# Kernel tuning notes

Hardware: AMD Instinct MI355X
Metric: run time of the kernel (lower is better)

Reference implementation:

```python
import jax, jax.numpy as jnp
import numpy as np

L = 2048      # seq_len
E = 2048      # hidden_dim
H = 16        # num_heads
D = E // H    # head_dim


def setup_inputs() -> dict:
    key = jax.random.key(0)
    ks = jax.random.split(key, 6)
    x = jax.random.normal(ks[0], (L, E), dtype=jnp.float32)
    bias_matrix = jax.random.normal(ks[1], (L, L), dtype=jnp.float32) * 0.1
    # nn.MultiheadAttention params: packed in_proj [3E, E] + bias [3E], out_proj [E, E] + bias [E]
    in_proj_weight = jax.random.normal(ks[2], (3 * E, E), dtype=jnp.float32) * 0.02
    in_proj_bias = jax.random.normal(ks[3], (3 * E,), dtype=jnp.float32) * 0.02
    out_proj_weight = jax.random.normal(ks[4], (E, E), dtype=jnp.float32) * 0.02
    out_proj_bias = jax.random.normal(ks[5], (E,), dtype=jnp.float32) * 0.02
    return {
        "x": x,
        "bias_matrix": bias_matrix,
        "in_proj_weight": in_proj_weight,
        "in_proj_bias": in_proj_bias,
        "out_proj_weight": out_proj_weight,
        "out_proj_bias": out_proj_bias,
    }


def reference(x, bias_matrix, in_proj_weight, in_proj_bias, out_proj_weight, out_proj_bias):
    # Packed QKV projection (torch Linear convention: y = x @ W.T + b)
    qkv = x @ in_proj_weight.T + in_proj_bias            # [L, 3E]
    q, k, v = jnp.split(qkv, 3, axis=-1)                 # each [L, E]
    q = q.reshape(L, H, D)
    k = k.reshape(L, H, D)
    v = v.reshape(L, H, D)
    scale = 1.0 / jnp.sqrt(jnp.asarray(D, dtype=x.dtype))
    # scores: [H, L, L]; bias_matrix broadcast over heads (torch 2D attn_mask semantics)
    scores = jnp.einsum("lhd,mhd->hlm", q * scale, k) + bias_matrix[None, :, :]
    attn = jax.nn.softmax(scores, axis=-1)
    ctx = jnp.einsum("hlm,mhd->lhd", attn, v).reshape(L, E)
    out = ctx @ out_proj_weight.T + out_proj_bias        # [L, E]
    return out
```

## Files before the change

### kernel.cpp

```cpp
#include <hip/hip_runtime.h>
#include <math.h>

#define L_SEQ 2048
#define E_DIM 2048
#define H_NUM 16
#define D_HEAD 128

typedef __attribute__((ext_vector_type(8))) _Float16 half8;
typedef __attribute__((ext_vector_type(4))) _Float16 half4;
typedef __attribute__((ext_vector_type(4))) float floatx4;

static __device__ __forceinline__ void gload16(const void* g, void* lds) {
  __builtin_amdgcn_global_load_lds(
      (const __attribute__((address_space(1))) void*)g,
      (__attribute__((address_space(3))) void*)lds, 16, 0, 0);
}

__global__ __launch_bounds__(256)
void cvt3_f32_f16(const float* __restrict__ a, _Float16* __restrict__ oa, int na,
                  const float* __restrict__ b, _Float16* __restrict__ ob, int nb,
                  const float* __restrict__ c, _Float16* __restrict__ oc, int nc) {
  int i = (blockIdx.x * 256 + threadIdx.x) * 8;
  const float* src;
  _Float16* dst;
  if (i < na) {
    src = a + i; dst = oa + i;
  } else if (i < na + nb) {
    src = b + (i - na); dst = ob + (i - na);
  } else if (i < na + nb + nc) {
    src = c + (i - na - nb); dst = oc + (i - na - nb);
  } else {
    return;
  }
  float4 p = *(const float4*)src;
  float4 q = *(const float4*)(src + 4);
  half8 h = {(_Float16)p.x, (_Float16)p.y, (_Float16)p.z, (_Float16)p.w,
             (_Float16)q.x, (_Float16)q.y, (_Float16)q.z, (_Float16)q.w};
  *(half8*)dst = h;
}

template <int TM, int TN, int WR, int WC, int EPI>
__global__ __launch_bounds__(256)
void gemm_mfma(const _Float16* __restrict__ A, const _Float16* __restrict__ B,
               const float* __restrict__ bias, float* __restrict__ C,
               _Float16* __restrict__ qk, _Float16* __restrict__ vt,
               int M, int N, int K) {
  constexpr int RT = TM / (16 * WR);
  constexpr int CT = TN / (16 * WC);
  constexpr int ACH = TM / 8;
  constexpr int NCH = (TM + TN) / 32;

  __shared__ _Float16 As[2][TM * 64];
  __shared__ _Float16 Bs[2][TN * 64];

  const int tid = threadIdx.x;
  const int wave = tid >> 6, lane = tid & 63;
  const int l15 = lane & 15, quad = lane >> 4;
  const int wr = wave / WC, wc = wave % WC;
  const int row0 = blockIdx.y * TM, col0 = blockIdx.x * TN;

  const int srow = lane >> 3;
  const int gc = (lane & 7) ^ srow;

  auto stage = [&](int buf, int k0) {
#pragma unroll
    for (int c = 0; c < NCH; ++c) {
      int chunk = wave * NCH + c;
      if (chunk < ACH) {
        int row = chunk * 8 + srow;
        gload16((const char*)(A + (size_t)(row0 + row) * K + k0) + gc * 16,
                (char*)&As[buf][0] + chunk * 1024);
      } else {
        int bch = chunk - ACH;
        int row = bch * 8 + srow;
        gload16((const char*)(B + (size_t)(col0 + row) * K + k0) + gc * 16,
                (char*)&Bs[buf][0] + bch * 1024);
      }
    }
  };

  floatx4 acc[RT][CT];
#pragma unroll
  for (int i = 0; i < RT; ++i)
#pragma unroll
    for (int j = 0; j < CT; ++j) acc[i][j] = (floatx4){0.f, 0.f, 0.f, 0.f};

  const int niter = K / 64;
  stage(0, 0);

  for (int it = 0; it < niter; ++it) {
    const int cur = it & 1;
    __syncthreads();
    if (it + 1 < niter) stage(cur ^ 1, (it + 1) * 64);

#pragma unroll
    for (int ks = 0; ks < 2; ++ks) {
      half8 af[RT], bf[CT];
#pragma unroll
      for (int t = 0; t < RT; ++t) {
        int r = wr * (16 * RT) + t * 16 + l15;
        af[t] = *(const half8*)&As[cur][r * 64 + (((ks * 4 + quad) ^ (r & 7)) * 8)];
      }
#pragma unroll
      for (int t = 0; t < CT; ++t) {
        int r = wc * (16 * CT) + t * 16 + l15;
        bf[t] = *(const half8*)&Bs[cur][r * 64 + (((ks * 4 + quad) ^ (r & 7)) * 8)];
      }
#pragma unroll
      for (int tr = 0; tr < RT; ++tr)
#pragma unroll
        for (int tc = 0; tc < CT; ++tc)
          acc[tr][tc] = __builtin_amdgcn_mfma_f32_16x16x32_f16(
              af[tr], bf[tc], acc[tr][tc], 0, 0, 0);
    }
  }

  const int crow = row0 + wr * (16 * RT);
  const int ccol = col0 + wc * (16 * CT);

  if (EPI == 0) {
#pragma unroll
    for (int tc = 0; tc < CT; ++tc) {
      int col = ccol + tc * 16 + l15;
      float bb = bias[col];
#pragma unroll
      for (int tr = 0; tr < RT; ++tr)
#pragma unroll
        for (int r = 0; r < 4; ++r)
          C[(size_t)(crow + tr * 16 + quad * 4 + r) * N + col] =
              acc[tr][tc][r] + bb;
    }
  } else if (col0 < 2 * E_DIM) {
#pragma unroll
    for (int tc = 0; tc < CT; ++tc) {
      int col = ccol + tc * 16 + l15;
      float bb = bias[col];
#pragma unroll
      for (int tr = 0; tr < RT; ++tr)
#pragma unroll
        for (int r = 0; r < 4; ++r)
          qk[(size_t)(crow + tr * 16 + quad * 4 + r) * (2 * E_DIM) + col] =
              (_Float16)(acc[tr][tc][r] + bb);
    }
  } else {
#pragma unroll
    for (int tc = 0; tc < CT; ++tc) {
      int col = ccol + tc * 16 + l15;
      float bb = bias[col];
      int vrow = col - 2 * E_DIM;
#pragma unroll
      for (int tr = 0; tr < RT; ++tr) {
        int rbase = crow + tr * 16 + quad * 4;
        half4 h = {(_Float16)(acc[tr][tc][0] + bb), (_Float16)(acc[tr][tc][1] + bb),
                   (_Float16)(acc[tr][tc][2] + bb), (_Float16)(acc[tr][tc][3] + bb)};
        *(half4*)&vt[(size_t)vrow * L_SEQ + rbase] = h;
      }
    }
  }
}

__global__ __launch_bounds__(256, 1)
void attn_mfma(const _Float16* __restrict__ qk, const _Float16* __restrict__ vt,
               const float* __restrict__ bias, _Float16* __restrict__ ctx) {
  const int h = blockIdx.x;
  const int q0 = blockIdx.y * 128;
  const int tid = threadIdx.x;
  const int wave = tid >> 6;
  const int lane = tid & 63;
  const int l15 = lane & 15;
  const int quad = lane >> 4;

  __shared__ _Float16 Ks[2][64][136];
  __shared__ _Float16 Vst[2][128][72];
  __shared__ _Float16 Ps[128][72];

  half8 qa[2][4];
#pragma unroll
  for (int rt = 0; rt < 2; ++rt) {
    const _Float16* qp = qk + (size_t)(q0 + wave * 32 + rt * 16 + l15) * (2 * E_DIM) +
                         h * D_HEAD + quad * 8;
#pragma unroll
    for (int ks = 0; ks < 4; ++ks) qa[rt][ks] = *(const half8*)(qp + ks * 32);
  }

  float l_i[2] = {0.f, 0.f};
  floatx4 o[2][8];
#pragma unroll
  for (int rt = 0; rt < 2; ++rt)
#pragma unroll
    for (int t = 0; t < 8; ++t) o[rt][t] = (floatx4){0.f, 0.f, 0.f, 0.f};

  const float scale = 0.088388347648318447f;

  half8 kreg[4], vreg[4];
  floatx4 bcur[2][4], bnxt[2][4];
#pragma unroll
  for (int c = 0; c < 4; ++c) {
    int m = c * 256 + tid;
    kreg[c] = *(const half8*)(qk + (size_t)(m >> 4) * (2 * E_DIM) + E_DIM +
                              h * D_HEAD + (m & 15) * 8);
    vreg[c] = *(const half8*)(vt + (size_t)(h * D_HEAD + (m >> 3)) * L_SEQ +
                              (m & 7) * 8);
  }
#pragma unroll
  for (int rt = 0; rt < 2; ++rt)
#pragma unroll
    for (int t = 0; t < 4; ++t)
      bcur[rt][t] = *(const floatx4*)&bias[(size_t)(q0 + wave * 32 + rt * 16 + l15) *
                                               L_SEQ + 16 * t + quad * 4];
#pragma unroll
  for (int c = 0; c < 4; ++c) {
    int m = c * 256 + tid;
    *(half8*)&Ks[0][m >> 4][(m & 15) * 8] = kreg[c];
    *(half8*)&Vst[0][m >> 3][(m & 7) * 8] = vreg[c];
  }

#pragma unroll 2
  for (int it = 0; it < 32; ++it) {
    const int cur = it & 1, nxt = cur ^ 1;
    const int kt = it * 64;
    __syncthreads();

    if (it < 31) {
#pragma unroll
      for (int c = 0; c < 4; ++c) {
        int m = c * 256 + tid;
        kreg[c] = *(const half8*)(qk + (size_t)(kt + 64 + (m >> 4)) * (2 * E_DIM) +
                                  E_DIM + h * D_HEAD + (m & 15) * 8);
        vreg[c] = *(const half8*)(vt + (size_t)(h * D_HEAD + (m >> 3)) * L_SEQ +
                                  kt + 64 + (m & 7) * 8);
      }
#pragma unroll
      for (int rt = 0; rt < 2; ++rt)
#pragma unroll
        for (int t = 0; t < 4; ++t)
          bnxt[rt][t] =
              *(const floatx4*)&bias[(size_t)(q0 + wave * 32 + rt * 16 + l15) *
                                         L_SEQ + kt + 64 + 16 * t + quad * 4];
    }

    floatx4 st[2][4];
#pragma unroll
    for (int t = 0; t < 4; ++t) {
      st[0][t] = (floatx4){0.f, 0.f, 0.f, 0.f};
      st[1][t] = (floatx4){0.f, 0.f, 0.f, 0.f};
    }
#pragma unroll
    for (int ks = 0; ks < 4; ++ks)
#pragma unroll
      for (int t = 0; t < 4; ++t) {
        half8 kf = *(const half8*)&Ks[cur][16 * t + l15][ks * 32 + quad * 8];
        st[0][t] = __builtin_amdgcn_mfma_f32_16x16x32_f16(kf, qa[0][ks], st[0][t], 0, 0, 0);
        st[1][t] = __builtin_amdgcn_mfma_f32_16x16x32_f16(kf, qa[1][ks], st[1][t], 0, 0, 0);
      }

#pragma unroll
    for (int rt = 0; rt < 2; ++rt) {
      float ls = 0.f;
      float ps[4][4];
#pragma unroll
      for (int t = 0; t < 4; ++t)
#pragma unroll
        for (int r = 0; r < 4; ++r) {
          float p = __expf(fmaf(st[rt][t][r], scale, bcur[rt][t][r]));
          ps[t][r] = p;
          ls += p;
        }
      ls += __shfl_xor(ls, 16);
      ls += __shfl_xor(ls, 32);
      l_i[rt] += ls;
#pragma unroll
      for (int t = 0; t < 4; ++t) {
        half4 hp = {(_Float16)ps[t][0], (_Float16)ps[t][1],
                    (_Float16)ps[t][2], (_Float16)ps[t][3]};
        *(half4*)&Ps[wave * 32 + rt * 16 + l15][16 * t + quad * 4] = hp;
      }
    }

    half8 pa[2][2];
#pragma unroll
    for (int rt = 0; rt < 2; ++rt)
#pragma unroll
      for (int ks = 0; ks < 2; ++ks)
        pa[rt][ks] = *(const half8*)&Ps[wave * 32 + rt * 16 + l15][ks * 32 + quad * 8];
#pragma unroll
    for (int t = 0; t < 8; ++t) {
#pragma unroll
      for (int ks = 0; ks < 2; ++ks) {
        half8 vf = *(const half8*)&Vst[cur][16 * t + l15][ks * 32 + quad * 8];
        o[0][t] = __builtin_amdgcn_mfma_f32_16x16x32_f16(pa[0][ks], vf, o[0][t], 0, 0, 0);
        o[1][t] = __builtin_amdgcn_mfma_f32_16x16x32_f16(pa[1][ks], vf, o[1][t], 0, 0, 0);
      }
    }

    if (it < 31) {
#pragma unroll
      for (int c = 0; c < 4; ++c) {
        int m = c * 256 + tid;
        *(half8*)&Ks[nxt][m >> 4][(m & 15) * 8] = kreg[c];
        *(half8*)&Vst[nxt][m >> 3][(m & 7) * 8] = vreg[c];
      }
#pragma unroll
      for (int rt = 0; rt < 2; ++rt)
#pragma unroll
        for (int t = 0; t < 4; ++t) bcur[rt][t] = bnxt[rt][t];
    }
  }

#pragma unroll
  for (int rt = 0; rt < 2; ++rt) {
    float inv[4];
#pragma unroll
    for (int r = 0; r < 4; ++r) inv[r] = 1.f / __shfl(l_i[rt], quad * 4 + r);
#pragma unroll
    for (int t = 0; t < 8; ++t)
#pragma unroll
      for (int r = 0; r < 4; ++r) {
        int row = q0 + wave * 32 + rt * 16 + quad * 4 + r;
        ctx[(size_t)row * E_DIM + h * D_HEAD + 16 * t + l15] =
            (_Float16)(o[rt][t][r] * inv[r]);
      }
  }
}

extern "C" void kernel_launch(void* const* d_in, const int* in_sizes, int n_in,
                              void* d_out, int out_size, void* d_ws, size_t ws_size,
                              hipStream_t stream) {
  const float* x          = (const float*)d_in[0];
  const float* bias_mat   = (const float*)d_in[1];
  const float* in_proj_w  = (const float*)d_in[2];
  const float* in_proj_b  = (const float*)d_in[3];
  const float* out_proj_w = (const float*)d_in[4];
  const float* out_proj_b = (const float*)d_in[5];
  float* out = (float*)d_out;

  _Float16* x16 = (_Float16*)d_ws;
  _Float16* w1  = x16 + (size_t)L_SEQ * E_DIM;
  _Float16* w2  = w1 + (size_t)3 * E_DIM * E_DIM;
  _Float16* qk  = w2 + (size_t)E_DIM * E_DIM;
  _Float16* vt  = qk + (size_t)L_SEQ * 2 * E_DIM;
  _Float16* ctx = vt + (size_t)E_DIM * L_SEQ;

  dim3 blk(256);
  const int nx = L_SEQ * E_DIM, nw1 = 3 * E_DIM * E_DIM, nw2 = E_DIM * E_DIM;

  cvt3_f32_f16<<<(nx + nw1 + nw2) / 2048, blk, 0, stream>>>(
      x, x16, nx, in_proj_w, w1, nw1, out_proj_w, w2, nw2);

  gemm_mfma<128, 128, 2, 2, 1><<<dim3(3 * E_DIM / 128, L_SEQ / 128), blk, 0, stream>>>(
      x16, w1, in_proj_b, nullptr, qk, vt, L_SEQ, 3 * E_DIM, E_DIM);

  attn_mfma<<<dim3(H_NUM, L_SEQ / 128), blk, 0, stream>>>(qk, vt, bias_mat, ctx);

  gemm_mfma<128, 64, 4, 1, 0><<<dim3(E_DIM / 64, L_SEQ / 128), blk, 0, stream>>>(
      ctx, w2, out_proj_b, out, nullptr, nullptr, L_SEQ, E_DIM, E_DIM);
}
```

Measured before the change: 285.4 us.

## Fuse fp32-to-fp16 conversion into GEMM loads and use 8-wave attention blocks

Drops the separate conversion kernel. The GEMMs now load fp32 inputs into registers and convert them to fp16 as they write to LDS, with the register loads prefetched across the MFMA loop. The attention kernel goes from 4 to 8 waves per block, each wave owning 16 query rows instead of 32, so more waves share each K/V tile. The cost is fp32 global reads of the weights inside the GEMM tiles (twice the bytes, read repeatedly across tiles) instead of a single conversion pass, and register-path staging in place of async direct-to-LDS loads.

```diff
diff --git a/kernel.cpp b/kernel.cpp
--- a/kernel.cpp
+++ b/kernel.cpp
@@ -16,32 +16,9 @@
       (__attribute__((address_space(3))) void*)lds, 16, 0, 0);
 }
 
-__global__ __launch_bounds__(256)
-void cvt3_f32_f16(const float* __restrict__ a, _Float16* __restrict__ oa, int na,
-                  const float* __restrict__ b, _Float16* __restrict__ ob, int nb,
-                  const float* __restrict__ c, _Float16* __restrict__ oc, int nc) {
-  int i = (blockIdx.x * 256 + threadIdx.x) * 8;
-  const float* src;
-  _Float16* dst;
-  if (i < na) {
-    src = a + i; dst = oa + i;
-  } else if (i < na + nb) {
-    src = b + (i - na); dst = ob + (i - na);
-  } else if (i < na + nb + nc) {
-    src = c + (i - na - nb); dst = oc + (i - na - nb);
-  } else {
-    return;
-  }
-  float4 p = *(const float4*)src;
-  float4 q = *(const float4*)(src + 4);
-  half8 h = {(_Float16)p.x, (_Float16)p.y, (_Float16)p.z, (_Float16)p.w,
-             (_Float16)q.x, (_Float16)q.y, (_Float16)q.z, (_Float16)q.w};
-  *(half8*)dst = h;
-}
-
-template <int TM, int TN, int WR, int WC, int EPI>
-__global__ __launch_bounds__(256)
-void gemm_mfma(const _Float16* __restrict__ A, const _Float16* __restrict__ B,
+template <int TM, int TN, int WR, int WC, int EPI, int CVTA, int CVTB>
+__global__ __launch_bounds__(256, 2)
+void gemm_mfma(const void* __restrict__ Ap, const void* __restrict__ Bp,
                const float* __restrict__ bias, float* __restrict__ C,
                _Float16* __restrict__ qk, _Float16* __restrict__ vt,
                int M, int N, int K) {
@@ -50,6 +27,11 @@
   constexpr int ACH = TM / 8;
   constexpr int NCH = (TM + TN) / 32;
 
+  const _Float16* A16 = (const _Float16*)Ap;
+  const float*    A32 = (const float*)Ap;
+  const _Float16* B16 = (const _Float16*)Bp;
+  const float*    B32 = (const float*)Bp;
+
   __shared__ _Float16 As[2][TM * 64];
   __shared__ _Float16 Bs[2][TN * 64];
 
@@ -62,22 +44,64 @@
   const int srow = lane >> 3;
   const int gc = (lane & 7) ^ srow;
 
-  auto stage = [&](int buf, int k0) {
+  float4 sreg[NCH][2];
+
+  auto loadRegs = [&](int k0) {
 #pragma unroll
     for (int c = 0; c < NCH; ++c) {
       int chunk = wave * NCH + c;
       if (chunk < ACH) {
-        int row = chunk * 8 + srow;
-        gload16((const char*)(A + (size_t)(row0 + row) * K + k0) + gc * 16,
-                (char*)&As[buf][0] + chunk * 1024);
+        if (CVTA) {
+          int row = chunk * 8 + srow;
+          const float* p = A32 + (size_t)(row0 + row) * K + k0 + gc * 8;
+          sreg[c][0] = *(const float4*)p;
+          sreg[c][1] = *(const float4*)(p + 4);
+        }
       } else {
-        int bch = chunk - ACH;
-        int row = bch * 8 + srow;
-        gload16((const char*)(B + (size_t)(col0 + row) * K + k0) + gc * 16,
-                (char*)&Bs[buf][0] + bch * 1024);
+        if (CVTB) {
+          int row = (chunk - ACH) * 8 + srow;
+          const float* p = B32 + (size_t)(col0 + row) * K + k0 + gc * 8;
+          sreg[c][0] = *(const float4*)p;
+          sreg[c][1] = *(const float4*)(p + 4);
+        }
       }
     }
   };
+  auto issueAsync = [&](int buf, int k0) {
+#pragma unroll
+    for (int c = 0; c < NCH; ++c) {
+      int chunk = wave * NCH + c;
+      if (chunk < ACH) {
+        if (!CVTA) {
+          int row = chunk * 8 + srow;
+          gload16((const char*)(A16 + (size_t)(row0 + row) * K + k0) + gc * 16,
+                  (char*)&As[buf][0] + chunk * 1024);
+        }
+      } else {
+        if (!CVTB) {
+          int row = (chunk - ACH) * 8 + srow;
+          gload16((const char*)(B16 + (size_t)(col0 + row) * K + k0) + gc * 16,
+                  (char*)&Bs[buf][0] + (chunk - ACH) * 1024);
+        }
+      }
+    }
+  };
+  auto writeRegs = [&](int buf) {
+#pragma unroll
+    for (int c = 0; c < NCH; ++c) {
+      int chunk = wave * NCH + c;
+      bool docvt = (chunk < ACH) ? (CVTA != 0) : (CVTB != 0);
+      if (docvt) {
+        float4 a = sreg[c][0], b = sreg[c][1];
+        half8 h = {(_Float16)a.x, (_Float16)a.y, (_Float16)a.z, (_Float16)a.w,
+                   (_Float16)b.x, (_Float16)b.y, (_Float16)b.z, (_Float16)b.w};
+        char* base = (chunk < ACH)
+                         ? (char*)&As[buf][0] + chunk * 1024
+                         : (char*)&Bs[buf][0] + (chunk - ACH) * 1024;
+        *(half8*)(base + lane * 16) = h;
+      }
+    }
+  };
 
   floatx4 acc[RT][CT];
 #pragma unroll
@@ -86,12 +110,17 @@
     for (int j = 0; j < CT; ++j) acc[i][j] = (floatx4){0.f, 0.f, 0.f, 0.f};
 
   const int niter = K / 64;
-  stage(0, 0);
+  loadRegs(0);
+  issueAsync(0, 0);
+  writeRegs(0);
 
   for (int it = 0; it < niter; ++it) {
     const int cur = it & 1;
     __syncthreads();
-    if (it + 1 < niter) stage(cur ^ 1, (it + 1) * 64);
+    if (it + 1 < niter) {
+      loadRegs((it + 1) * 64);
+      issueAsync(cur ^ 1, (it + 1) * 64);
+    }
 
 #pragma unroll
     for (int ks = 0; ks < 2; ++ks) {
@@ -113,6 +142,8 @@
           acc[tr][tc] = __builtin_amdgcn_mfma_f32_16x16x32_f16(
               af[tr], bf[tc], acc[tr][tc], 0, 0, 0);
     }
+
+    if (it + 1 < niter) writeRegs(cur ^ 1);
   }
 
   const int crow = row0 + wr * (16 * RT);
@@ -159,7 +190,7 @@
   }
 }
 
-__global__ __launch_bounds__(256, 1)
+__global__ __launch_bounds__(512, 2)
 void attn_mfma(const _Float16* __restrict__ qk, const _Float16* __restrict__ vt,
                const float* __restrict__ bias, _Float16* __restrict__ ctx) {
   const int h = blockIdx.x;
@@ -174,43 +205,38 @@
   __shared__ _Float16 Vst[2][128][72];
   __shared__ _Float16 Ps[128][72];
 
-  half8 qa[2][4];
-#pragma unroll
-  for (int rt = 0; rt < 2; ++rt) {
-    const _Float16* qp = qk + (size_t)(q0 + wave * 32 + rt * 16 + l15) * (2 * E_DIM) +
+  half8 qa[4];
+  {
+    const _Float16* qp = qk + (size_t)(q0 + wave * 16 + l15) * (2 * E_DIM) +
                          h * D_HEAD + quad * 8;
 #pragma unroll
-    for (int ks = 0; ks < 4; ++ks) qa[rt][ks] = *(const half8*)(qp + ks * 32);
-  }
-
-  float l_i[2] = {0.f, 0.f};
-  floatx4 o[2][8];
-#pragma unroll
-  for (int rt = 0; rt < 2; ++rt)
-#pragma unroll
-    for (int t = 0; t < 8; ++t) o[rt][t] = (floatx4){0.f, 0.f, 0.f, 0.f};
+    for (int ks = 0; ks < 4; ++ks) qa[ks] = *(const half8*)(qp + ks * 32);
+  }
+
+  float l_i = 0.f;
+  floatx4 o[8];
+#pragma unroll
+  for (int t = 0; t < 8; ++t) o[t] = (floatx4){0.f, 0.f, 0.f, 0.f};
 
   const float scale = 0.088388347648318447f;
 
-  half8 kreg[4], vreg[4];
-  floatx4 bcur[2][4], bnxt[2][4];
-#pragma unroll
-  for (int c = 0; c < 4; ++c) {
-    int m = c * 256 + tid;
+  half8 kreg[2], vreg[2];
+  floatx4 bcur[4], bnxt[4];
+#pragma unroll
+  for (int c = 0; c < 2; ++c) {
+    int m = c * 512 + tid;
     kreg[c] = *(const half8*)(qk + (size_t)(m >> 4) * (2 * E_DIM) + E_DIM +
                               h * D_HEAD + (m & 15) * 8);
     vreg[c] = *(const half8*)(vt + (size_t)(h * D_HEAD + (m >> 3)) * L_SEQ +
                               (m & 7) * 8);
   }
 #pragma unroll
-  for (int rt = 0; rt < 2; ++rt)
-#pragma unroll
-    for (int t = 0; t < 4; ++t)
-      bcur[rt][t] = *(const floatx4*)&bias[(size_t)(q0 + wave * 32 + rt * 16 + l15) *
-                                               L_SEQ + 16 * t + quad * 4];
-#pragma unroll
-  for (int c = 0; c < 4; ++c) {
-    int m = c * 256 + tid;
+  for (int t = 0; t < 4; ++t)
+    bcur[t] = *(const floatx4*)&bias[(size_t)(q0 + wave * 16 + l15) * L_SEQ +
+                                    16 * t + quad * 4];
+#pragma unroll
+  for (int c = 0; c < 2; ++c) {
+    int m = c * 512 + tid;
     *(half8*)&Ks[0][m >> 4][(m & 15) * 8] = kreg[c];
     *(half8*)&Vst[0][m >> 3][(m & 7) * 8] = vreg[c];
   }
@@ -223,104 +249,87 @@
 
     if (it < 31) {
 #pragma unroll
-      for (int c = 0; c < 4; ++c) {
-        int m = c * 256 + tid;
+      for (int c = 0; c < 2; ++c) {
+        int m = c * 512 + tid;
         kreg[c] = *(const half8*)(qk + (size_t)(kt + 64 + (m >> 4)) * (2 * E_DIM) +
                                   E_DIM + h * D_HEAD + (m & 15) * 8);
         vreg[c] = *(const half8*)(vt + (size_t)(h * D_HEAD + (m >> 3)) * L_SEQ +
                                   kt + 64 + (m & 7) * 8);
       }
 #pragma unroll
-      for (int rt = 0; rt < 2; ++rt)
-#pragma unroll
-        for (int t = 0; t < 4; ++t)
-          bnxt[rt][t] =
-              *(const floatx4*)&bias[(size_t)(q0 + wave * 32 + rt * 16 + l15) *
-                                         L_SEQ + kt + 64 + 16 * t + quad * 4];
-    }
-
-    floatx4 st[2][4];
-#pragma unroll
-    for (int t = 0; t < 4; ++t) {
-      st[0][t] = (floatx4){0.f, 0.f, 0.f, 0.f};
-      st[1][t] = (floatx4){0.f, 0.f, 0.f, 0.f};
-    }
+      for (int t = 0; t < 4; ++t)
+        bnxt[t] = *(const floatx4*)&bias[(size_t)(q0 + wave * 16 + l15) * L_SEQ +
+                                         kt + 64 + 16 * t + quad * 4];
+    }
+
+    floatx4 st[4];
+#pragma unroll
+    for (int t = 0; t < 4; ++t) st[t] = (floatx4){0.f, 0.f, 0.f, 0.f};
 #pragma unroll
     for (int ks = 0; ks < 4; ++ks)
 #pragma unroll
       for (int t = 0; t < 4; ++t) {
         half8 kf = *(const half8*)&Ks[cur][16 * t + l15][ks * 32 + quad * 8];
-        st[0][t] = __builtin_amdgcn_mfma_f32_16x16x32_f16(kf, qa[0][ks], st[0][t], 0, 0, 0);
-        st[1][t] = __builtin_amdgcn_mfma_f32_16x16x32_f16(kf, qa[1][ks], st[1][t], 0, 0, 0);
-      }
-
-#pragma unroll
-    for (int rt = 0; rt < 2; ++rt) {
+        st[t] = __builtin_amdgcn_mfma_f32_16x16x32_f16(kf, qa[ks], st[t], 0, 0, 0);
+      }
+
+    {
       float ls = 0.f;
       float ps[4][4];
 #pragma unroll
       for (int t = 0; t < 4; ++t)
 #pragma unroll
         for (int r = 0; r < 4; ++r) {
-          float p = __expf(fmaf(st[rt][t][r], scale, bcur[rt][t][r]));
+          float p = __expf(fmaf(st[t][r], scale, bcur[t][r]));
           ps[t][r] = p;
           ls += p;
         }
       ls += __shfl_xor(ls, 16);
       ls += __shfl_xor(ls, 32);
-      l_i[rt] += ls;
+      l_i += ls;
 #pragma unroll
       for (int t = 0; t < 4; ++t) {
         half4 hp = {(_Float16)ps[t][0], (_Float16)ps[t][1],
                     (_Float16)ps[t][2], (_Float16)ps[t][3]};
-        *(half4*)&Ps[wave * 32 + rt * 16 + l15][16 * t + quad * 4] = hp;
-      }
-    }
-
-    half8 pa[2][2];
-#pragma unroll
-    for (int rt = 0; rt < 2; ++rt)
-#pragma unroll
-      for (int ks = 0; ks < 2; ++ks)
-        pa[rt][ks] = *(const half8*)&Ps[wave * 32 + rt * 16 + l15][ks * 32 + quad * 8];
-#pragma unroll
-    for (int t = 0; t < 8; ++t) {
+        *(half4*)&Ps[wave * 16 + l15][16 * t + quad * 4] = hp;
+      }
+    }
+
+    half8 pa[2];
+#pragma unroll
+    for (int ks = 0; ks < 2; ++ks)
+      pa[ks] = *(const half8*)&Ps[wave * 16 + l15][ks * 32 + quad * 8];
+#pragma unroll
+    for (int t = 0; t < 8; ++t)
 #pragma unroll
       for (int ks = 0; ks < 2; ++ks) {
         half8 vf = *(const half8*)&Vst[cur][16 * t + l15][ks * 32 + quad * 8];
-        o[0][t] = __builtin_amdgcn_mfma_f32_16x16x32_f16(pa[0][ks], vf, o[0][t], 0, 0, 0);
-        o[1][t] = __builtin_amdgcn_mfma_f32_16x16x32_f16(pa[1][ks], vf, o[1][t], 0, 0, 0);
-      }
-    }
+        o[t] = __builtin_amdgcn_mfma_f32_16x16x32_f16(pa[ks], vf, o[t], 0, 0, 0);
+      }
 
     if (it < 31) {
 #pragma unroll
-      for (int c = 0; c < 4; ++c) {
-        int m = c * 256 + tid;
+      for (int c = 0; c < 2; ++c) {
+        int m = c * 512 + tid;
         *(half8*)&Ks[nxt][m >> 4][(m & 15) * 8] = kreg[c];
         *(half8*)&Vst[nxt][m >> 3][(m & 7) * 8] = vreg[c];
       }
 #pragma unroll
-      for (int rt = 0; rt < 2; ++rt)
-#pragma unroll
-        for (int t = 0; t < 4; ++t) bcur[rt][t] = bnxt[rt][t];
-    }
-  }
-
-#pragma unroll
-  for (int rt = 0; rt < 2; ++rt) {
-    float inv[4];
-#pragma unroll
-    for (int r = 0; r < 4; ++r) inv[r] = 1.f / __shfl(l_i[rt], quad * 4 + r);
-#pragma unroll
-    for (int t = 0; t < 8; ++t)
-#pragma unroll
-      for (int r = 0; r < 4; ++r) {
-        int row = q0 + wave * 32 + rt * 16 + quad * 4 + r;
-        ctx[(size_t)row * E_DIM + h * D_HEAD + 16 * t + l15] =
-            (_Float16)(o[rt][t][r] * inv[r]);
-      }
-  }
+      for (int t = 0; t < 4; ++t) bcur[t] = bnxt[t];
+    }
+  }
+
+  float inv[4];
+#pragma unroll
+  for (int r = 0; r < 4; ++r) inv[r] = 1.f / __shfl(l_i, quad * 4 + r);
+#pragma unroll
+  for (int t = 0; t < 8; ++t)
+#pragma unroll
+    for (int r = 0; r < 4; ++r) {
+      int row = q0 + wave * 16 + quad * 4 + r;
+      ctx[(size_t)row * E_DIM + h * D_HEAD + 16 * t + l15] =
+          (_Float16)(o[t][r] * inv[r]);
+    }
 }
 
 extern "C" void kernel_launch(void* const* d_in, const int* in_sizes, int n_in,
@@ -334,24 +343,18 @@
   const float* out_proj_b = (const float*)d_in[5];
   float* out = (float*)d_out;
 
-  _Float16* x16 = (_Float16*)d_ws;
-  _Float16* w1  = x16 + (size_t)L_SEQ * E_DIM;
-  _Float16* w2  = w1 + (size_t)3 * E_DIM * E_DIM;
-  _Float16* qk  = w2 + (size_t)E_DIM * E_DIM;
+  _Float16* qk  = (_Float16*)d_ws;
   _Float16* vt  = qk + (size_t)L_SEQ * 2 * E_DIM;
   _Float16* ctx = vt + (size_t)E_DIM * L_SEQ;
 
-  dim3 blk(256);
-  const int nx = L_SEQ * E_DIM, nw1 = 3 * E_DIM * E_DIM, nw2 = E_DIM * E_DIM;
-
-  cvt3_f32_f16<<<(nx + nw1 + nw2) / 2048, blk, 0, stream>>>(
-      x, x16, nx, in_proj_w, w1, nw1, out_proj_w, w2, nw2);
-
-  gemm_mfma<128, 128, 2, 2, 1><<<dim3(3 * E_DIM / 128, L_SEQ / 128), blk, 0, stream>>>(
-      x16, w1, in_proj_b, nullptr, qk, vt, L_SEQ, 3 * E_DIM, E_DIM);
-
-  attn_mfma<<<dim3(H_NUM, L_SEQ / 128), blk, 0, stream>>>(qk, vt, bias_mat, ctx);
-
-  gemm_mfma<128, 64, 4, 1, 0><<<dim3(E_DIM / 64, L_SEQ / 128), blk, 0, stream>>>(
-      ctx, w2, out_proj_b, out, nullptr, nullptr, L_SEQ, E_DIM, E_DIM);
+  gemm_mfma<128, 128, 2, 2, 1, 1, 1>
+      <<<dim3(3 * E_DIM / 128, L_SEQ / 128), dim3(256), 0, stream>>>(
+          x, in_proj_w, in_proj_b, nullptr, qk, vt, L_SEQ, 3 * E_DIM, E_DIM);
+
+  attn_mfma<<<dim3(H_NUM, L_SEQ / 128), dim3(512), 0, stream>>>(qk, vt, bias_mat,
+                                                                ctx);
+
+  gemm_mfma<128, 64, 4, 1, 0, 0, 1>
+      <<<dim3(E_DIM / 64, L_SEQ / 128), dim3(256), 0, stream>>>(
+          ctx, out_proj_w, out_proj_b, out, nullptr, nullptr, L_SEQ, E_DIM, E_DIM);
 }
```

New measurement: 319.2 us. 1.12x slower.

## Use 8 waves per attention block, 16 query rows per wave

Applied to the files above, without the earlier changes.

Changes the attention kernel from 4 waves handling 32 query rows each to 8 waves handling 16 rows each, launched with 512 threads and launch bounds allowing 2 blocks per CU. K/V tile loads are split across twice as many threads. The aim is more waves resident per CU to hide memory and exp latency, plus fewer registers per thread. The cost is that each K/V fragment read from LDS now feeds only one MFMA instead of two, so LDS traffic per FLOP doubles.

```diff
diff --git a/kernel.cpp b/kernel.cpp
--- a/kernel.cpp
+++ b/kernel.cpp
@@ -159,7 +159,7 @@
   }
 }
 
-__global__ __launch_bounds__(256, 1)
+__global__ __launch_bounds__(512, 2)
 void attn_mfma(const _Float16* __restrict__ qk, const _Float16* __restrict__ vt,
                const float* __restrict__ bias, _Float16* __restrict__ ctx) {
   const int h = blockIdx.x;
@@ -174,43 +174,38 @@
   __shared__ _Float16 Vst[2][128][72];
   __shared__ _Float16 Ps[128][72];
 
-  half8 qa[2][4];
-#pragma unroll
-  for (int rt = 0; rt < 2; ++rt) {
-    const _Float16* qp = qk + (size_t)(q0 + wave * 32 + rt * 16 + l15) * (2 * E_DIM) +
+  half8 qa[4];
+  {
+    const _Float16* qp = qk + (size_t)(q0 + wave * 16 + l15) * (2 * E_DIM) +
                          h * D_HEAD + quad * 8;
 #pragma unroll
-    for (int ks = 0; ks < 4; ++ks) qa[rt][ks] = *(const half8*)(qp + ks * 32);
-  }
-
-  float l_i[2] = {0.f, 0.f};
-  floatx4 o[2][8];
-#pragma unroll
-  for (int rt = 0; rt < 2; ++rt)
-#pragma unroll
-    for (int t = 0; t < 8; ++t) o[rt][t] = (floatx4){0.f, 0.f, 0.f, 0.f};
+    for (int ks = 0; ks < 4; ++ks) qa[ks] = *(const half8*)(qp + ks * 32);
+  }
+
+  float l_i = 0.f;
+  floatx4 o[8];
+#pragma unroll
+  for (int t = 0; t < 8; ++t) o[t] = (floatx4){0.f, 0.f, 0.f, 0.f};
 
   const float scale = 0.088388347648318447f;
 
-  half8 kreg[4], vreg[4];
-  floatx4 bcur[2][4], bnxt[2][4];
-#pragma unroll
-  for (int c = 0; c < 4; ++c) {
-    int m = c * 256 + tid;
+  half8 kreg[2], vreg[2];
+  floatx4 bcur[4], bnxt[4];
+#pragma unroll
+  for (int c = 0; c < 2; ++c) {
+    int m = c * 512 + tid;
     kreg[c] = *(const half8*)(qk + (size_t)(m >> 4) * (2 * E_DIM) + E_DIM +
                               h * D_HEAD + (m & 15) * 8);
     vreg[c] = *(const half8*)(vt + (size_t)(h * D_HEAD + (m >> 3)) * L_SEQ +
                               (m & 7) * 8);
   }
 #pragma unroll
-  for (int rt = 0; rt < 2; ++rt)
-#pragma unroll
-    for (int t = 0; t < 4; ++t)
-      bcur[rt][t] = *(const floatx4*)&bias[(size_t)(q0 + wave * 32 + rt * 16 + l15) *
-                                               L_SEQ + 16 * t + quad * 4];
-#pragma unroll
-  for (int c = 0; c < 4; ++c) {
-    int m = c * 256 + tid;
+  for (int t = 0; t < 4; ++t)
+    bcur[t] = *(const floatx4*)&bias[(size_t)(q0 + wave * 16 + l15) * L_SEQ +
+                                    16 * t + quad * 4];
+#pragma unroll
+  for (int c = 0; c < 2; ++c) {
+    int m = c * 512 + tid;
     *(half8*)&Ks[0][m >> 4][(m & 15) * 8] = kreg[c];
     *(half8*)&Vst[0][m >> 3][(m & 7) * 8] = vreg[c];
   }
@@ -223,104 +218,87 @@
 
     if (it < 31) {
 #pragma unroll
-      for (int c = 0; c < 4; ++c) {
-        int m = c * 256 + tid;
+      for (int c = 0; c < 2; ++c) {
+        int m = c * 512 + tid;
         kreg[c] = *(const half8*)(qk + (size_t)(kt + 64 + (m >> 4)) * (2 * E_DIM) +
                                   E_DIM + h * D_HEAD + (m & 15) * 8);
         vreg[c] = *(const half8*)(vt + (size_t)(h * D_HEAD + (m >> 3)) * L_SEQ +
                                   kt + 64 + (m & 7) * 8);
       }
 #pragma unroll
-      for (int rt = 0; rt < 2; ++rt)
-#pragma unroll
-        for (int t = 0; t < 4; ++t)
-          bnxt[rt][t] =
-              *(const floatx4*)&bias[(size_t)(q0 + wave * 32 + rt * 16 + l15) *
-                                         L_SEQ + kt + 64 + 16 * t + quad * 4];
-    }
-
-    floatx4 st[2][4];
-#pragma unroll
-    for (int t = 0; t < 4; ++t) {
-      st[0][t] = (floatx4){0.f, 0.f, 0.f, 0.f};
-      st[1][t] = (floatx4){0.f, 0.f, 0.f, 0.f};
-    }
+      for (int t = 0; t < 4; ++t)
+        bnxt[t] = *(const floatx4*)&bias[(size_t)(q0 + wave * 16 + l15) * L_SEQ +
+                                         kt + 64 + 16 * t + quad * 4];
+    }
+
+    floatx4 st[4];
+#pragma unroll
+    for (int t = 0; t < 4; ++t) st[t] = (floatx4){0.f, 0.f, 0.f, 0.f};
 #pragma unroll
     for (int ks = 0; ks < 4; ++ks)
 #pragma unroll
       for (int t = 0; t < 4; ++t) {
         half8 kf = *(const half8*)&Ks[cur][16 * t + l15][ks * 32 + quad * 8];
-        st[0][t] = __builtin_amdgcn_mfma_f32_16x16x32_f16(kf, qa[0][ks], st[0][t], 0, 0, 0);
-        st[1][t] = __builtin_amdgcn_mfma_f32_16x16x32_f16(kf, qa[1][ks], st[1][t], 0, 0, 0);
-      }
-
-#pragma unroll
-    for (int rt = 0; rt < 2; ++rt) {
+        st[t] = __builtin_amdgcn_mfma_f32_16x16x32_f16(kf, qa[ks], st[t], 0, 0, 0);
+      }
+
+    {
       float ls = 0.f;
       float ps[4][4];
 #pragma unroll
       for (int t = 0; t < 4; ++t)
 #pragma unroll
         for (int r = 0; r < 4; ++r) {
-          float p = __expf(fmaf(st[rt][t][r], scale, bcur[rt][t][r]));
+          float p = __expf(fmaf(st[t][r], scale, bcur[t][r]));
           ps[t][r] = p;
           ls += p;
         }
       ls += __shfl_xor(ls, 16);
       ls += __shfl_xor(ls, 32);
-      l_i[rt] += ls;
+      l_i += ls;
 #pragma unroll
       for (int t = 0; t < 4; ++t) {
         half4 hp = {(_Float16)ps[t][0], (_Float16)ps[t][1],
                     (_Float16)ps[t][2], (_Float16)ps[t][3]};
-        *(half4*)&Ps[wave * 32 + rt * 16 + l15][16 * t + quad * 4] = hp;
-      }
-    }
-
-    half8 pa[2][2];
-#pragma unroll
-    for (int rt = 0; rt < 2; ++rt)
-#pragma unroll
-      for (int ks = 0; ks < 2; ++ks)
-        pa[rt][ks] = *(const half8*)&Ps[wave * 32 + rt * 16 + l15][ks * 32 + quad * 8];
-#pragma unroll
-    for (int t = 0; t < 8; ++t) {
+        *(half4*)&Ps[wave * 16 + l15][16 * t + quad * 4] = hp;
+      }
+    }
+
+    half8 pa[2];
+#pragma unroll
+    for (int ks = 0; ks < 2; ++ks)
+      pa[ks] = *(const half8*)&Ps[wave * 16 + l15][ks * 32 + quad * 8];
+#pragma unroll
+    for (int t = 0; t < 8; ++t)
 #pragma unroll
       for (int ks = 0; ks < 2; ++ks) {
         half8 vf = *(const half8*)&Vst[cur][16 * t + l15][ks * 32 + quad * 8];
-        o[0][t] = __builtin_amdgcn_mfma_f32_16x16x32_f16(pa[0][ks], vf, o[0][t], 0, 0, 0);
-        o[1][t] = __builtin_amdgcn_mfma_f32_16x16x32_f16(pa[1][ks], vf, o[1][t], 0, 0, 0);
-      }
-    }
+        o[t] = __builtin_amdgcn_mfma_f32_16x16x32_f16(pa[ks], vf, o[t], 0, 0, 0);
+      }
 
     if (it < 31) {
 #pragma unroll
-      for (int c = 0; c < 4; ++c) {
-        int m = c * 256 + tid;
+      for (int c = 0; c < 2; ++c) {
+        int m = c * 512 + tid;
         *(half8*)&Ks[nxt][m >> 4][(m & 15) * 8] = kreg[c];
         *(half8*)&Vst[nxt][m >> 3][(m & 7) * 8] = vreg[c];
       }
 #pragma unroll
-      for (int rt = 0; rt < 2; ++rt)
-#pragma unroll
-        for (int t = 0; t < 4; ++t) bcur[rt][t] = bnxt[rt][t];
-    }
-  }
-
-#pragma unroll
-  for (int rt = 0; rt < 2; ++rt) {
-    float inv[4];
-#pragma unroll
-    for (int r = 0; r < 4; ++r) inv[r] = 1.f / __shfl(l_i[rt], quad * 4 + r);
-#pragma unroll
-    for (int t = 0; t < 8; ++t)
-#pragma unroll
-      for (int r = 0; r < 4; ++r) {
-        int row = q0 + wave * 32 + rt * 16 + quad * 4 + r;
-        ctx[(size_t)row * E_DIM + h * D_HEAD + 16 * t + l15] =
-            (_Float16)(o[rt][t][r] * inv[r]);
-      }
-  }
+      for (int t = 0; t < 4; ++t) bcur[t] = bnxt[t];
+    }
+  }
+
+  float inv[4];
+#pragma unroll
+  for (int r = 0; r < 4; ++r) inv[r] = 1.f / __shfl(l_i, quad * 4 + r);
+#pragma unroll
+  for (int t = 0; t < 8; ++t)
+#pragma unroll
+    for (int r = 0; r < 4; ++r) {
+      int row = q0 + wave * 16 + quad * 4 + r;
+      ctx[(size_t)row * E_DIM + h * D_HEAD + 16 * t + l15] =
+          (_Float16)(o[t][r] * inv[r]);
+    }
 }
 
 extern "C" void kernel_launch(void* const* d_in, const int* in_sizes, int n_in,
@@ -350,7 +328,8 @@
   gemm_mfma<128, 128, 2, 2, 1><<<dim3(3 * E_DIM / 128, L_SEQ / 128), blk, 0, stream>>>(
       x16, w1, in_proj_b, nullptr, qk, vt, L_SEQ, 3 * E_DIM, E_DIM);
 
-  attn_mfma<<<dim3(H_NUM, L_SEQ / 128), blk, 0, stream>>>(qk, vt, bias_mat, ctx);
+  attn_mfma<<<dim3(H_NUM, L_SEQ / 128), dim3(512), 0, stream>>>(qk, vt, bias_mat,
+                                                                ctx);
 
   gemm_mfma<128, 64, 4, 1, 0><<<dim3(E_DIM / 64, L_SEQ / 128), blk, 0, stream>>>(
       ctx, w2, out_proj_b, out, nullptr, nullptr, L_SEQ, E_DIM, E_DIM);
```

After: 284.4 us. Within noise of the previous version (-0.3%).
